# Performance work log

Hardware: AMD Instinct MI355X
Metric: run time of the kernel (lower is better)

The kernel has to match this reference:

```python
import jax, jax.numpy as jnp
import numpy as np

NUM_STEPS = 150  # module default; tsize bins spanning [-1, 1]
N, D, NUM_CLASSES = 4096, 512, 64


def setup_inputs() -> dict:
    key = jax.random.key(0)
    kf, kc = jax.random.split(key)
    feats = jax.random.normal(kf, (N, D), dtype=jnp.float32)
    # HistogramLoss assumes similarities in [-1, 1] -> L2-normalize embeddings
    feats = feats / jnp.linalg.norm(feats, axis=1, keepdims=True)
    classes = jax.random.randint(kc, (N,), 0, NUM_CLASSES, dtype=jnp.int64)
    return {"features": feats, "classes": classes}


def reference(features, classes):
    step = 2.0 / (NUM_STEPS - 1)
    n = features.shape[0]

    # pairwise cosine similarities
    dists = features @ features.T  # [N, N]

    # upper-triangle (i < j) pair selector and class-equality masks
    triu = jnp.triu(jnp.ones((n, n), dtype=bool), 1)
    eq = classes[:, None] == classes[None, :]
    pos_w = (triu & eq).astype(dists.dtype)
    neg_w = (triu & ~eq).astype(dists.dtype)

    # soft linear binning: each similarity contributes (1-frac) to bin idx
    # and frac to bin idx+1 (equivalent to the torch delta/t equality masks)
    idx = jnp.clip(jnp.floor((dists + 1.0) / step), 0, NUM_STEPS - 1).astype(jnp.int32)
    delta = idx.astype(dists.dtype) * step - 1.0  # quantized lower bin edge
    frac = (dists - delta) / step
    idx1 = jnp.minimum(idx + 1, NUM_STEPS - 1)

    def hist(w):
        h = jnp.zeros((NUM_STEPS,), dtype=dists.dtype)
        h = h.at[idx].add((1.0 - frac) * w)
        h = h.at[idx1].add(frac * w)
        return h

    hist_pos = hist(pos_w) / jnp.sum(pos_w)
    hist_neg = hist(neg_w) / jnp.sum(neg_w)

    # CDF of positives (tril-masked sum == cumulative sum), then overlap loss
    cdf_pos = jnp.cumsum(hist_pos)
    loss = jnp.sum(hist_neg * cdf_pos)
    return loss
```

## Files before the change

### kernel.cpp

```cpp
#include <hip/hip_runtime.h>
#include <hip/hip_bf16.h>
#include <stdint.h>

#define N_PTS 4096
#define DIMS  512
#define NBINS 150
#define NREP  8
#define HSTRIDE 9
#define NTILES 528

typedef short bf16x8 __attribute__((ext_vector_type(8)));
typedef float f32x4  __attribute__((ext_vector_type(4)));

#define AS_G(p) ((const __attribute__((address_space(1))) void*)(p))
#define AS_L(p) ((__attribute__((address_space(3))) void*)(p))

__device__ __forceinline__ unsigned short f2bf(float f) {
  union { float f; unsigned int u; } v; v.f = f;
  unsigned int u = v.u;
  return (unsigned short)((u + 0x7FFFu + ((u >> 16) & 1u)) >> 16);
}

__device__ __forceinline__ float gload_agent(const float* p) {
  return __hip_atomic_load(p, __ATOMIC_RELAXED, __HIP_MEMORY_SCOPE_AGENT);
}

__global__ void convert_kernel(const float* __restrict__ in,
                               unsigned short* __restrict__ out,
                               float* __restrict__ acc_g) {
  int t = blockIdx.x * blockDim.x + threadIdx.x;
  float4 v = ((const float4*)in)[t];
  ushort4 o;
  o.x = f2bf(v.x); o.y = f2bf(v.y); o.z = f2bf(v.z); o.w = f2bf(v.w);
  ((ushort4*)out)[t] = o;
  if (t < 4 * NBINS + 4) acc_g[t] = 0.0f;
}

__global__ void __launch_bounds__(256) fused_kernel(
    const unsigned short* __restrict__ fb,
    const int* __restrict__ cls,
    float* __restrict__ acc_g,
    float* __restrict__ out) {
  int t = blockIdx.x, bi = 0;
  while (t >= 32 - bi) { t -= 32 - bi; ++bi; }
  const int bj = bi + t;

  __shared__ __align__(16) short lds_a[128 * 64];
  __shared__ __align__(16) short lds_b[128 * 64];
  __shared__ unsigned int lds_hist[2 * NBINS * HSTRIDE];
  __shared__ int lds_cls[256];
  __shared__ unsigned int last_flag;

  const int tid  = threadIdx.x;
  const int wave = tid >> 6, lane = tid & 63;
  const int wm = wave >> 1, wn = wave & 1;
  const int m16 = lane & 15, quad = lane >> 4;
  const int rep = lane & 7;

  for (int i = tid; i < 2 * NBINS * HSTRIDE; i += 256) lds_hist[i] = 0u;
  {
    int base = (tid < 128 ? bi : bj) * 128;
    lds_cls[tid] = cls[base + (tid & 127)];
  }

  const int lrow  = lane >> 3;
  const int lslot = (lane & 7) ^ lrow;
  const size_t rowA0 = (size_t)bi * 128, rowB0 = (size_t)bj * 128;

  f32x4 acc[4][4];
#pragma unroll
  for (int a = 0; a < 4; ++a)
#pragma unroll
    for (int b = 0; b < 4; ++b) acc[a][b] = (f32x4){0.f, 0.f, 0.f, 0.f};

  for (int k0 = 0; k0 < DIMS; k0 += 64) {
    __syncthreads();
#pragma unroll
    for (int c = 0; c < 4; ++c) {
      int inst = wave * 4 + c;
      int row  = inst * 8 + lrow;
      const unsigned short* ga = fb + (rowA0 + row) * DIMS + k0 + lslot * 8;
      const unsigned short* gb = fb + (rowB0 + row) * DIMS + k0 + lslot * 8;
      __builtin_amdgcn_global_load_lds(AS_G(ga), AS_L(&lds_a[inst * 512]), 16, 0, 0);
      __builtin_amdgcn_global_load_lds(AS_G(gb), AS_L(&lds_b[inst * 512]), 16, 0, 0);
    }
    __syncthreads();

#pragma unroll
    for (int ks = 0; ks < 2; ++ks) {
      bf16x8 af[4], bv[4];
      const int q = ks * 4 + quad;
#pragma unroll
      for (int f = 0; f < 4; ++f) {
        int ra = wm * 64 + f * 16 + m16;
        af[f] = *(const bf16x8*)&lds_a[ra * 64 + ((q ^ (ra & 7)) * 8)];
        int rb = wn * 64 + f * 16 + m16;
        bv[f] = *(const bf16x8*)&lds_b[rb * 64 + ((q ^ (rb & 7)) * 8)];
      }
#pragma unroll
      for (int fm = 0; fm < 4; ++fm)
#pragma unroll
        for (int fn = 0; fn < 4; ++fn)
          acc[fm][fn] = __builtin_amdgcn_mfma_f32_16x16x32_bf16(
              af[fm], bv[fn], acc[fm][fn], 0, 0, 0);
    }
  }

  const bool diag = (bi == bj);
  int cj[4], ci[4][4];
#pragma unroll
  for (int fn = 0; fn < 4; ++fn) cj[fn] = lds_cls[128 + wn * 64 + fn * 16 + m16];
#pragma unroll
  for (int fm = 0; fm < 4; ++fm)
#pragma unroll
    for (int r = 0; r < 4; ++r)
      ci[fm][r] = lds_cls[wm * 64 + fm * 16 + quad * 4 + r];

#pragma unroll
  for (int fm = 0; fm < 4; ++fm) {
#pragma unroll
    for (int fn = 0; fn < 4; ++fn) {
#pragma unroll
      for (int r = 0; r < 4; ++r) {
        int i_loc = wm * 64 + fm * 16 + quad * 4 + r;
        int j_loc = wn * 64 + fn * 16 + m16;
        if (diag && j_loc <= i_loc) continue;
        float d = acc[fm][fn][r];
        float x = fmaxf(fmaf(d, 74.5f, 74.5f), 0.0f);
        int idx = (int)x;
        idx = idx > NBINS - 1 ? NBINS - 1 : idx;
        float frac = x - (float)idx;
        unsigned int fx = (unsigned int)fmaf(frac, 4096.0f, 0.5f);
        unsigned int packed = (1u << 22) + fx;
        int sel = (ci[fm][r] == cj[fn]) ? 0 : 1;
        unsigned int off = (unsigned int)(sel * (NBINS * HSTRIDE) + idx * HSTRIDE + rep);
        __hip_atomic_fetch_add(&lds_hist[off], packed,
                               __ATOMIC_RELAXED, __HIP_MEMORY_SCOPE_WORKGROUP);
      }
    }
  }

  __syncthreads();
  for (int e = tid; e < 2 * NBINS; e += 256) {
    unsigned int cnt = 0, fs = 0;
    const unsigned int* h = &lds_hist[e * HSTRIDE];
#pragma unroll
    for (int rp = 0; rp < NREP; ++rp) {
      unsigned int v = h[rp];
      cnt += v >> 22;
      fs  += v & 0x3FFFFFu;
    }
    if (cnt) {
      unsafeAtomicAdd(&acc_g[e], (float)cnt);
      unsafeAtomicAdd(&acc_g[2 * NBINS + e], (float)fs);
    }
  }

  __syncthreads();
  if (tid == 0) {
    __threadfence();
    unsigned int prev = atomicAdd((unsigned int*)(acc_g + 4 * NBINS), 1u);
    last_flag = (prev == NTILES - 1) ? 1u : 0u;
  }
  __syncthreads();
  if (last_flag && tid < 64) {
    __threadfence();
    const float is = 1.0f / 4096.0f;
    const float* cntp = acc_g;
    const float* fsp  = acc_g + 2 * NBINS;
    float sp = 0.f, sn = 0.f;
#pragma unroll
    for (int rr = 0; rr < 3; ++rr) {
      int b = rr * 64 + lane;
      if (b < NBINS) {
        sp += gload_agent(cntp + b);
        sn += gload_agent(cntp + NBINS + b);
      }
    }
#pragma unroll
    for (int o = 32; o; o >>= 1) { sp += __shfl_xor(sp, o); sn += __shfl_xor(sn, o); }
    float carry = 0.f, pf0 = 0.f, pf1 = 0.f, lacc = 0.f;
#pragma unroll
    for (int rr = 0; rr < 3; ++rr) {
      int b = rr * 64 + lane;
      bool ok = b < NBINS;
      float c0 = ok ? gload_agent(cntp + b) : 0.f;
      float f0 = ok ? gload_agent(fsp + b) : 0.f;
      float c1 = ok ? gload_agent(cntp + NBINS + b) : 0.f;
      float f1 = ok ? gload_agent(fsp + NBINS + b) : 0.f;
      float f0m1 = __shfl_up(f0, 1); if (lane == 0) f0m1 = pf0;
      float f1m1 = __shfl_up(f1, 1); if (lane == 0) f1m1 = pf1;
      float hp = ok ? (c0 + (f0m1 - f0) * is) : 0.f;
      float hn = ok ? (c1 + (f1m1 - f1) * is) : 0.f;
      if (b == NBINS - 1) { hp += f0 * is; hn += f1 * is; }
      float s = hp;
#pragma unroll
      for (int o = 1; o < 64; o <<= 1) {
        float u = __shfl_up(s, o);
        if (lane >= o) s += u;
      }
      if (ok) lacc += hn * ((carry + s) / sp);
      carry += __shfl(s, 63);
      pf0 = __shfl(f0, 63); pf1 = __shfl(f1, 63);
    }
#pragma unroll
    for (int o = 32; o; o >>= 1) lacc += __shfl_xor(lacc, o);
    if (lane == 0) out[0] = lacc / sn;
  }
}

extern "C" void kernel_launch(void* const* d_in, const int* in_sizes, int n_in,
                              void* d_out, int out_size, void* d_ws, size_t ws_size,
                              hipStream_t stream) {
  const float* feats   = (const float*)d_in[0];
  const int*   classes = (const int*)d_in[1];
  unsigned short* fb   = (unsigned short*)d_ws;
  float* acc_g = (float*)((char*)d_ws + (size_t)N_PTS * DIMS * 2);
  float* out   = (float*)d_out;

  hipLaunchKernelGGL(convert_kernel, dim3((N_PTS * DIMS / 4) / 256), dim3(256), 0, stream,
                     feats, fb, acc_g);
  hipLaunchKernelGGL(fused_kernel, dim3(NTILES), dim3(256), 0, stream,
                     fb, classes, acc_g, out);
}
```

Baseline: 97.02 us.

## Replicate global histogram accumulators and halve LDS histogram replicas

Splits the global float accumulator into 16 replicas indexed by block id, so the 528 tiles spread their atomic adds across copies instead of all hitting one set of addresses. The last block sums the replicas into LDS before doing the CDF/loss reduction. It also cuts the per-bin LDS replicas from 8 to 4, which shrinks the LDS histogram but can raise same-address atomic contention. A launch-bounds occupancy hint of 4 blocks per CU is added.

```diff
diff --git a/kernel.cpp b/kernel.cpp
--- a/kernel.cpp
+++ b/kernel.cpp
@@ -5,8 +5,9 @@
 #define N_PTS 4096
 #define DIMS  512
 #define NBINS 150
-#define NREP  8
-#define HSTRIDE 9
+#define NREP  4
+#define HSTRIDE 5
+#define GREP  16
 #define NTILES 528
 
 typedef short bf16x8 __attribute__((ext_vector_type(8)));
@@ -33,10 +34,10 @@
   ushort4 o;
   o.x = f2bf(v.x); o.y = f2bf(v.y); o.z = f2bf(v.z); o.w = f2bf(v.w);
   ((ushort4*)out)[t] = o;
-  if (t < 4 * NBINS + 4) acc_g[t] = 0.0f;
-}
-
-__global__ void __launch_bounds__(256) fused_kernel(
+  if (t < GREP * 4 * NBINS + 4) acc_g[t] = 0.0f;
+}
+
+__global__ void __launch_bounds__(256, 4) fused_kernel(
     const unsigned short* __restrict__ fb,
     const int* __restrict__ cls,
     float* __restrict__ acc_g,
@@ -55,7 +56,7 @@
   const int wave = tid >> 6, lane = tid & 63;
   const int wm = wave >> 1, wn = wave & 1;
   const int m16 = lane & 15, quad = lane >> 4;
-  const int rep = lane & 7;
+  const int rep = lane & (NREP - 1);
 
   for (int i = tid; i < 2 * NBINS * HSTRIDE; i += 256) lds_hist[i] = 0u;
   {
@@ -141,6 +142,7 @@
   }
 
   __syncthreads();
+  float* myacc = acc_g + (blockIdx.x & (GREP - 1)) * (4 * NBINS);
   for (int e = tid; e < 2 * NBINS; e += 256) {
     unsigned int cnt = 0, fs = 0;
     const unsigned int* h = &lds_hist[e * HSTRIDE];
@@ -151,61 +153,69 @@
       fs  += v & 0x3FFFFFu;
     }
     if (cnt) {
-      unsafeAtomicAdd(&acc_g[e], (float)cnt);
-      unsafeAtomicAdd(&acc_g[2 * NBINS + e], (float)fs);
+      unsafeAtomicAdd(&myacc[e], (float)cnt);
+      unsafeAtomicAdd(&myacc[2 * NBINS + e], (float)fs);
     }
   }
 
   __syncthreads();
   if (tid == 0) {
     __threadfence();
-    unsigned int prev = atomicAdd((unsigned int*)(acc_g + 4 * NBINS), 1u);
+    unsigned int prev = atomicAdd((unsigned int*)(acc_g + GREP * 4 * NBINS), 1u);
     last_flag = (prev == NTILES - 1) ? 1u : 0u;
   }
   __syncthreads();
-  if (last_flag && tid < 64) {
+  if (last_flag) {
     __threadfence();
-    const float is = 1.0f / 4096.0f;
-    const float* cntp = acc_g;
-    const float* fsp  = acc_g + 2 * NBINS;
-    float sp = 0.f, sn = 0.f;
-#pragma unroll
-    for (int rr = 0; rr < 3; ++rr) {
-      int b = rr * 64 + lane;
-      if (b < NBINS) {
-        sp += gload_agent(cntp + b);
-        sn += gload_agent(cntp + NBINS + b);
-      }
-    }
-#pragma unroll
-    for (int o = 32; o; o >>= 1) { sp += __shfl_xor(sp, o); sn += __shfl_xor(sn, o); }
-    float carry = 0.f, pf0 = 0.f, pf1 = 0.f, lacc = 0.f;
-#pragma unroll
-    for (int rr = 0; rr < 3; ++rr) {
-      int b = rr * 64 + lane;
-      bool ok = b < NBINS;
-      float c0 = ok ? gload_agent(cntp + b) : 0.f;
-      float f0 = ok ? gload_agent(fsp + b) : 0.f;
-      float c1 = ok ? gload_agent(cntp + NBINS + b) : 0.f;
-      float f1 = ok ? gload_agent(fsp + NBINS + b) : 0.f;
-      float f0m1 = __shfl_up(f0, 1); if (lane == 0) f0m1 = pf0;
-      float f1m1 = __shfl_up(f1, 1); if (lane == 0) f1m1 = pf1;
-      float hp = ok ? (c0 + (f0m1 - f0) * is) : 0.f;
-      float hn = ok ? (c1 + (f1m1 - f1) * is) : 0.f;
-      if (b == NBINS - 1) { hp += f0 * is; hn += f1 * is; }
-      float s = hp;
-#pragma unroll
-      for (int o = 1; o < 64; o <<= 1) {
-        float u = __shfl_up(s, o);
-        if (lane >= o) s += u;
-      }
-      if (ok) lacc += hn * ((carry + s) / sp);
-      carry += __shfl(s, 63);
-      pf0 = __shfl(f0, 63); pf1 = __shfl(f1, 63);
-    }
-#pragma unroll
-    for (int o = 32; o; o >>= 1) lacc += __shfl_xor(lacc, o);
-    if (lane == 0) out[0] = lacc / sn;
+    float* fin = (float*)lds_hist;
+    for (int e = tid; e < 4 * NBINS; e += 256) {
+      float s = 0.f;
+#pragma unroll
+      for (int rp = 0; rp < GREP; ++rp)
+        s += gload_agent(acc_g + rp * (4 * NBINS) + e);
+      fin[e] = s;
+    }
+    __syncthreads();
+    if (tid < 64) {
+      const float is = 1.0f / 4096.0f;
+      const float* cntp = fin;
+      const float* fsp  = fin + 2 * NBINS;
+      float sp = 0.f, sn = 0.f;
+#pragma unroll
+      for (int rr = 0; rr < 3; ++rr) {
+        int b = rr * 64 + lane;
+        if (b < NBINS) { sp += cntp[b]; sn += cntp[NBINS + b]; }
+      }
+#pragma unroll
+      for (int o = 32; o; o >>= 1) { sp += __shfl_xor(sp, o); sn += __shfl_xor(sn, o); }
+      float carry = 0.f, pf0 = 0.f, pf1 = 0.f, lacc = 0.f;
+#pragma unroll
+      for (int rr = 0; rr < 3; ++rr) {
+        int b = rr * 64 + lane;
+        bool ok = b < NBINS;
+        float c0 = ok ? cntp[b] : 0.f;
+        float f0 = ok ? fsp[b] : 0.f;
+        float c1 = ok ? cntp[NBINS + b] : 0.f;
+        float f1 = ok ? fsp[NBINS + b] : 0.f;
+        float f0m1 = __shfl_up(f0, 1); if (lane == 0) f0m1 = pf0;
+        float f1m1 = __shfl_up(f1, 1); if (lane == 0) f1m1 = pf1;
+        float hp = ok ? (c0 + (f0m1 - f0) * is) : 0.f;
+        float hn = ok ? (c1 + (f1m1 - f1) * is) : 0.f;
+        if (b == NBINS - 1) { hp += f0 * is; hn += f1 * is; }
+        float s = hp;
+#pragma unroll
+        for (int o = 1; o < 64; o <<= 1) {
+          float u = __shfl_up(s, o);
+          if (lane >= o) s += u;
+        }
+        if (ok) lacc += hn * ((carry + s) / sp);
+        carry += __shfl(s, 63);
+        pf0 = __shfl(f0, 63); pf1 = __shfl(f1, 63);
+      }
+#pragma unroll
+      for (int o = 32; o; o >>= 1) lacc += __shfl_xor(lacc, o);
+      if (lane == 0) out[0] = lacc / sn;
+    }
   }
 }
 
```

Result: faster. 85.92 us (-11.4%).
